# Kernel tuning notes

Measured on AMD Instinct MI355X. Metric: run time of the kernel, lower is better.

## Reference

```python
import jax, jax.numpy as jnp
import numpy as np

B, L, D, H = 4, 2048, 1024, 16
HD = D // H  # head dim = 64


def setup_inputs() -> dict:
    key = jax.random.key(0)
    ks = jax.random.split(key, 8)
    std_qkv = np.sqrt(D + D // H).astype(np.float32)  # matches nn.init.normal_ std in source
    xav = np.sqrt(2.0 / (D + D)).astype(np.float32)   # xavier_normal_ for fc_out
    return {
        "query": jax.random.normal(ks[0], (B, L, D), dtype=jnp.float32),
        "key": jax.random.normal(ks[1], (B, L, D), dtype=jnp.float32),
        "value": jax.random.normal(ks[2], (B, L, D), dtype=jnp.float32),
        "Wq": jax.random.normal(ks[3], (D, D), dtype=jnp.float32) * std_qkv,
        "Wk": jax.random.normal(ks[4], (D, D), dtype=jnp.float32) * std_qkv,
        "Wv": jax.random.normal(ks[5], (D, D), dtype=jnp.float32) * std_qkv,
        "Wo": jax.random.normal(ks[6], (D, D), dtype=jnp.float32) * xav,
        "bo": jnp.zeros((D,), dtype=jnp.float32),
    }


def reference(query, key, value, Wq, Wk, Wv, Wo, bo):
    # Linear projections (torch Linear: x @ W.T), then split heads: b l (h k) -> b h l k
    def split_heads(x):
        b, l, _ = x.shape
        return x.reshape(b, l, H, HD).transpose(0, 2, 1, 3)

    q = split_heads(query @ Wq.T)   # [B,H,L,HD]
    k = split_heads(key @ Wk.T)     # [B,H,T,HD]
    v = split_heads(value @ Wv.T)   # [B,H,T,HD]

    scale = 1.0 / np.sqrt(HD).astype(np.float32)
    energy = jnp.einsum("bhlk,bhtk->bhlt", q, k) * scale  # [B,H,L,T]
    attention = jax.nn.softmax(energy, axis=3)
    out = jnp.einsum("bhlt,bhtv->bhlv", attention, v)     # [B,H,L,HD]
    # b h l v -> b l (h v)
    out = out.transpose(0, 2, 1, 3).reshape(B, L, D)
    out = out @ Wo.T + bo  # dropout_rate=0.0 -> identity
    return out, attention
```

## Files before the change

### kernel.cpp

```cpp
#include <hip/hip_runtime.h>
#include <math.h>

#define Bb 4
#define Ls 2048
#define Dd 1024
#define Hh 16
#define HDm 64
#define ML (Bb*Ls)

typedef double f64x4 __attribute__((ext_vector_type(4)));
typedef unsigned int u32;

__device__ __forceinline__ void gload16(const void* g, void* l) {
  __builtin_amdgcn_global_load_lds(
      (const __attribute__((address_space(1))) u32*)g,
      (__attribute__((address_space(3))) u32*)l, 16, 0, 0);
}

__global__ __launch_bounds__(256) void gemm_nt_mfma_f64(
    const float* __restrict__ A, const float* __restrict__ B,
    double* __restrict__ C, double outscale) {
  const int N = Dd, K = Dd;
  __shared__ float As[64][17];
  __shared__ float Bs[64][17];
  const int tid = threadIdx.x;
  const int lane = tid & 63;
  const int w = tid >> 6;
  const int lrow = lane & 15, lk = lane >> 4;
  const int bm = blockIdx.y * 64, bn = blockIdx.x * 64;
  const int sr = tid >> 4, sc = tid & 15;

  f64x4 acc[4] = {{0.,0.,0.,0.},{0.,0.,0.,0.},{0.,0.,0.,0.},{0.,0.,0.,0.}};

  for (int k0 = 0; k0 < K; k0 += 16) {
#pragma unroll
    for (int i = 0; i < 4; i++) {
      int r = sr + 16 * i;
      As[r][sc] = A[(size_t)(bm + r) * K + k0 + sc];
      Bs[r][sc] = B[(size_t)(bn + r) * K + k0 + sc];
    }
    __syncthreads();
#pragma unroll
    for (int t = 0; t < 4; t++) {
      double a = (double)As[16 * w + lrow][4 * t + lk];
#pragma unroll
      for (int j = 0; j < 4; j++) {
        double bb = (double)Bs[16 * j + lrow][4 * t + lk];
        acc[j] = __builtin_amdgcn_mfma_f64_16x16x4f64(a, bb, acc[j], 0, 0, 0);
      }
    }
    __syncthreads();
  }
#pragma unroll
  for (int j = 0; j < 4; j++)
#pragma unroll
    for (int d = 0; d < 4; d++) {
      size_t m = (size_t)(bm + 16 * w + 4 * d + lk);
      C[m * N + bn + 16 * j + lrow] = acc[j][d] * outscale;
    }
}

__global__ __launch_bounds__(256) void gemm_nt_mfma_f32(
    const float* __restrict__ A, const float* __restrict__ B,
    const float* __restrict__ bias, float* __restrict__ C) {
  const int N = Dd, K = Dd;
  __shared__ float As[64][17];
  __shared__ float Bs[64][17];
  const int tid = threadIdx.x;
  const int lane = tid & 63;
  const int w = tid >> 6;
  const int lrow = lane & 15, lk = lane >> 4;
  const int bm = blockIdx.y * 64, bn = blockIdx.x * 64;
  const int sr = tid >> 4, sc = tid & 15;

  f64x4 acc[4] = {{0.,0.,0.,0.},{0.,0.,0.,0.},{0.,0.,0.,0.},{0.,0.,0.,0.}};

  for (int k0 = 0; k0 < K; k0 += 16) {
#pragma unroll
    for (int i = 0; i < 4; i++) {
      int r = sr + 16 * i;
      As[r][sc] = A[(size_t)(bm + r) * K + k0 + sc];
      Bs[r][sc] = B[(size_t)(bn + r) * K + k0 + sc];
    }
    __syncthreads();
#pragma unroll
    for (int t = 0; t < 4; t++) {
      double a = (double)As[16 * w + lrow][4 * t + lk];
#pragma unroll
      for (int j = 0; j < 4; j++) {
        double bb = (double)Bs[16 * j + lrow][4 * t + lk];
        acc[j] = __builtin_amdgcn_mfma_f64_16x16x4f64(a, bb, acc[j], 0, 0, 0);
      }
    }
    __syncthreads();
  }
#pragma unroll
  for (int j = 0; j < 4; j++)
#pragma unroll
    for (int d = 0; d < 4; d++) {
      size_t m = (size_t)(bm + 16 * w + 4 * d + lk);
      int n = bn + 16 * j + lrow;
      float v = (float)acc[j][d];
      if (bias) v += bias[n];
      C[m * N + n] = v;
    }
}

__global__ __launch_bounds__(256) void attn_flash(
    double* __restrict__ Qd, const double* __restrict__ Kd,
    const float* __restrict__ Vf, float* __restrict__ attn,
    float* __restrict__ O) {
  __shared__ double Kbuf[2][32 * 64];
  __shared__ float  Vbuf[2][32 * 64];
  __shared__ float  Ps[4][32 * 20];

  const int tid = threadIdx.x;
  const int lane = tid & 63;
  const int w = tid >> 6;
  const int lrow = lane & 15;
  const int lk = lane >> 4;
  const int blk = blockIdx.x;
  const int qt = blk & 31;
  const int h = (blk >> 5) & 15;
  const int b = blk >> 9;
  const int l0 = qt * 64;

  const double* Qg = Qd + ((size_t)(b * Ls + l0)) * Dd + h * HDm;
  const double* Kg = Kd + ((size_t)b * Ls) * Dd + h * HDm;
  const float*  Vg = Vf + ((size_t)b * Ls) * Dd + h * HDm;
  float* aout = attn + ((size_t)((b * Hh + h) * Ls + l0)) * Ls;

  double qreg[16];
#pragma unroll
  for (int t = 0; t < 16; t++)
    qreg[t] = Qg[(size_t)(16 * w + lrow) * Dd + 4 * t + lk];

  const int l16 = (lane & 31) * 16;
  const int halfk = lane >> 5;
  const int vin = (lane & 15) * 16;
  const int vrow = lane >> 4;
  const int sx = (lrow & 7) << 1;

  auto stage = [&](int kts, int bsel) {
#pragma unroll
    for (int jj = 0; jj < 4; jj++) {
      int i = w + 4 * jj;
      int row = 2 * i + halfk;
      int inner = l16 ^ ((row & 7) << 4);
      const char* g = (const char*)Kg + (((size_t)(kts * 32 + row)) << 13) + inner;
      gload16(g, (char*)(&Kbuf[bsel][0]) + i * 1024);
    }
#pragma unroll
    for (int jj = 0; jj < 2; jj++) {
      int j = w + 4 * jj;
      int row = 4 * j + vrow;
      const char* g = (const char*)Vg + (((size_t)(kts * 32 + row)) << 12) + vin;
      gload16(g, (char*)(&Vbuf[bsel][0]) + j * 1024);
    }
  };

  float mreff[4];
  double sacc[4];
  float Oacc[4][4];
#pragma unroll
  for (int d = 0; d < 4; d++) {
    mreff[d] = -INFINITY;
    sacc[d] = 0.0;
#pragma unroll
    for (int j = 0; j < 4; j++) Oacc[d][j] = 0.0f;
  }

  stage(0, 0);
  __syncthreads();

  int cur = 0;
  for (int kt = 0; kt < 64; kt++) {
    if (kt < 63) stage(kt + 1, cur ^ 1);

    const double* Kb = &Kbuf[cur][0];
    const float*  Vb = &Vbuf[cur][0];

    f64x4 acc0 = {0.0, 0.0, 0.0, 0.0};
    f64x4 acc1 = {0.0, 0.0, 0.0, 0.0};
#pragma unroll
    for (int t = 0; t < 16; t++) {
      int ko = (4 * t + lk) ^ sx;
      double b0 = Kb[lrow * 64 + ko];
      double b1 = Kb[(16 + lrow) * 64 + ko];
      acc0 = __builtin_amdgcn_mfma_f64_16x16x4f64(qreg[t], b0, acc0, 0, 0, 0);
      acc1 = __builtin_amdgcn_mfma_f64_16x16x4f64(qreg[t], b1, acc1, 0, 0, 0);
    }

#pragma unroll
    for (int d = 0; d < 4; d++) {
      double e0 = acc0[d];
      double e1 = acc1[d];
      float tmf = fmaxf((float)e0, (float)e1);
#pragma unroll
      for (int m = 1; m < 16; m <<= 1) tmf = fmaxf(tmf, __shfl_xor(tmf, m));
      float mo_f = mreff[d];
      float ref_f = fmaxf(mo_f, tmf);
      double ref = (double)ref_f;
      float p0 = expf((float)(e0 - ref));
      float p1 = expf((float)(e1 - ref));
      double ts = (double)p0 + (double)p1;
#pragma unroll
      for (int m = 1; m < 16; m <<= 1) ts += __shfl_xor(ts, m);
      float factor = expf(mo_f - ref_f);
      sacc[d] = sacc[d] * (double)factor + ts;
      mreff[d] = ref_f;
#pragma unroll
      for (int j = 0; j < 4; j++) Oacc[d][j] *= factor;
      int row = 16 * w + 4 * d + lk;
      aout[(size_t)row * Ls + kt * 32 + lrow] = p0;
      aout[(size_t)row * Ls + kt * 32 + 16 + lrow] = p1;
      if (lrow == 0) {
        ((float*)(Qd + ((size_t)(b * Ls + l0 + row)) * Dd + h * HDm))[kt] = ref_f;
      }
      Ps[w][lrow * 20 + 4 * lk + d] = p0;
      Ps[w][(16 + lrow) * 20 + 4 * lk + d] = p1;
    }

#pragma unroll
    for (int t = 0; t < 32; t++) {
      float4 pb = *(const float4*)(&Ps[w][t * 20 + 4 * lk]);
      float4 vv = *(const float4*)(&Vb[t * 64 + lrow * 4]);
      Oacc[0][0] = fmaf(pb.x, vv.x, Oacc[0][0]);
      Oacc[0][1] = fmaf(pb.x, vv.y, Oacc[0][1]);
      Oacc[0][2] = fmaf(pb.x, vv.z, Oacc[0][2]);
      Oacc[0][3] = fmaf(pb.x, vv.w, Oacc[0][3]);
      Oacc[1][0] = fmaf(pb.y, vv.x, Oacc[1][0]);
      Oacc[1][1] = fmaf(pb.y, vv.y, Oacc[1][1]);
      Oacc[1][2] = fmaf(pb.y, vv.z, Oacc[1][2]);
      Oacc[1][3] = fmaf(pb.y, vv.w, Oacc[1][3]);
      Oacc[2][0] = fmaf(pb.z, vv.x, Oacc[2][0]);
      Oacc[2][1] = fmaf(pb.z, vv.y, Oacc[2][1]);
      Oacc[2][2] = fmaf(pb.z, vv.z, Oacc[2][2]);
      Oacc[2][3] = fmaf(pb.z, vv.w, Oacc[2][3]);
      Oacc[3][0] = fmaf(pb.w, vv.x, Oacc[3][0]);
      Oacc[3][1] = fmaf(pb.w, vv.y, Oacc[3][1]);
      Oacc[3][2] = fmaf(pb.w, vv.z, Oacc[3][2]);
      Oacc[3][3] = fmaf(pb.w, vv.w, Oacc[3][3]);
    }

    __syncthreads();
    cur ^= 1;
  }

#pragma unroll
  for (int d = 0; d < 4; d++) {
    int row = 16 * w + 4 * d + lk;
    float sv = (float)(1.0 / sacc[d]);
    float4 ov = make_float4(Oacc[d][0] * sv, Oacc[d][1] * sv,
                            Oacc[d][2] * sv, Oacc[d][3] * sv);
    *(float4*)(O + ((size_t)(b * Ls + l0 + row)) * Dd + h * HDm + lrow * 4) = ov;
    if (lrow == 0) {
      float* mrow = (float*)(Qd + ((size_t)(b * Ls + l0 + row)) * Dd + h * HDm);
      mrow[64] = mreff[d];
      *(double*)(mrow + 66) = sacc[d];
    }
  }
}

__global__ __launch_bounds__(256) void attn_scale(
    float* __restrict__ attn, const double* __restrict__ Qd) {
  int R = blockIdx.x;
  int b = R >> 15;
  int rem = R & 32767;
  int h = rem >> 11;
  int l = rem & 2047;
  const float* mrow = (const float*)(Qd + ((size_t)(b * Ls + l)) * Dd + h * HDm);
  int tid = threadIdx.x;
  int kt = tid >> 2;
  double mt = (double)mrow[kt];
  double mf = (double)mrow[64];
  double s = *(const double*)(mrow + 66);
  float sc = (float)(exp(mt - mf) / s);
  float4* ap = (float4*)(attn + (size_t)R * Ls + tid * 8);
  float4 a0 = ap[0], a1 = ap[1];
  a0.x *= sc; a0.y *= sc; a0.z *= sc; a0.w *= sc;
  a1.x *= sc; a1.y *= sc; a1.z *= sc; a1.w *= sc;
  ap[0] = a0; ap[1] = a1;
}

extern "C" void kernel_launch(void* const* d_in, const int* in_sizes, int n_in,
                              void* d_out, int out_size, void* d_ws, size_t ws_size,
                              hipStream_t stream) {
  const float* query = (const float*)d_in[0];
  const float* key   = (const float*)d_in[1];
  const float* value = (const float*)d_in[2];
  const float* Wq    = (const float*)d_in[3];
  const float* Wk    = (const float*)d_in[4];
  const float* Wv    = (const float*)d_in[5];
  const float* Wo    = (const float*)d_in[6];
  const float* bo    = (const float*)d_in[7];

  float* out0 = (float*)d_out;
  float* attn = out0 + (size_t)ML * Dd;

  char* ws = (char*)d_ws;
  double* Qd = (double*)ws;
  double* Kd = (double*)(ws + (size_t)ML * Dd * 8);
  float*  Vf = (float*)(ws + (size_t)ML * Dd * 16);
  float*  Of = (float*)(ws + (size_t)ML * Dd * 16 + (size_t)ML * Dd * 4);

  dim3 gemm_grid(Dd / 64, ML / 64);
  gemm_nt_mfma_f64<<<gemm_grid, 256, 0, stream>>>(query, Wq, Qd, 0.125);
  gemm_nt_mfma_f64<<<gemm_grid, 256, 0, stream>>>(key,   Wk, Kd, 1.0);
  gemm_nt_mfma_f32<<<gemm_grid, 256, 0, stream>>>(value, Wv, nullptr, Vf);

  attn_flash<<<Bb * Hh * (Ls / 64), 256, 0, stream>>>(Qd, Kd, Vf, attn, Of);
  attn_scale<<<Bb * Hh * Ls, 256, 0, stream>>>(attn, Qd);

  gemm_nt_mfma_f32<<<gemm_grid, 256, 0, stream>>>(Of, Wo, bo, out0);
}
```

Baseline: 4.203 ms.

## Compute P·V with bf16 MFMA using bf16-stored V projection

The V projection now writes its output as bf16 instead of fp32, and the attention kernel's P·V product moves from scalar FMA loops to bf16 16x16x32 MFMA instructions. P is packed to bf16 in shared memory, and the per-row rescale factors pass through a small shared buffer. This is meant to cut VALU work and V load bandwidth in the flash loop. In exchange it lowers the precision of V and P in the output accumulation, and it reads the V fragment with strided scalar LDS loads.

```diff
diff --git a/kernel.cpp b/kernel.cpp
--- a/kernel.cpp
+++ b/kernel.cpp
@@ -9,12 +9,21 @@
 #define ML (Bb*Ls)
 
 typedef double f64x4 __attribute__((ext_vector_type(4)));
+typedef float  f32x4 __attribute__((ext_vector_type(4)));
+typedef short  bf16x8 __attribute__((ext_vector_type(8)));
 typedef unsigned int u32;
+typedef unsigned short u16;
 
 __device__ __forceinline__ void gload16(const void* g, void* l) {
   __builtin_amdgcn_global_load_lds(
       (const __attribute__((address_space(1))) u32*)g,
       (__attribute__((address_space(3))) u32*)l, 16, 0, 0);
+}
+
+__device__ __forceinline__ u16 f2bf(float f) {
+  u32 u = __float_as_uint(f);
+  u += 0x7FFFu + ((u >> 16) & 1u);
+  return (u16)(u >> 16);
 }
 
 __global__ __launch_bounds__(256) void gemm_nt_mfma_f64(
@@ -106,13 +115,57 @@
     }
 }
 
+__global__ __launch_bounds__(256) void gemm_nt_mfma_bf16o(
+    const float* __restrict__ A, const float* __restrict__ B,
+    u16* __restrict__ C) {
+  const int N = Dd, K = Dd;
+  __shared__ float As[64][17];
+  __shared__ float Bs[64][17];
+  const int tid = threadIdx.x;
+  const int lane = tid & 63;
+  const int w = tid >> 6;
+  const int lrow = lane & 15, lk = lane >> 4;
+  const int bm = blockIdx.y * 64, bn = blockIdx.x * 64;
+  const int sr = tid >> 4, sc = tid & 15;
+
+  f64x4 acc[4] = {{0.,0.,0.,0.},{0.,0.,0.,0.},{0.,0.,0.,0.},{0.,0.,0.,0.}};
+
+  for (int k0 = 0; k0 < K; k0 += 16) {
+#pragma unroll
+    for (int i = 0; i < 4; i++) {
+      int r = sr + 16 * i;
+      As[r][sc] = A[(size_t)(bm + r) * K + k0 + sc];
+      Bs[r][sc] = B[(size_t)(bn + r) * K + k0 + sc];
+    }
+    __syncthreads();
+#pragma unroll
+    for (int t = 0; t < 4; t++) {
+      double a = (double)As[16 * w + lrow][4 * t + lk];
+#pragma unroll
+      for (int j = 0; j < 4; j++) {
+        double bb = (double)Bs[16 * j + lrow][4 * t + lk];
+        acc[j] = __builtin_amdgcn_mfma_f64_16x16x4f64(a, bb, acc[j], 0, 0, 0);
+      }
+    }
+    __syncthreads();
+  }
+#pragma unroll
+  for (int j = 0; j < 4; j++)
+#pragma unroll
+    for (int d = 0; d < 4; d++) {
+      size_t m = (size_t)(bm + 16 * w + 4 * d + lk);
+      C[m * N + bn + 16 * j + lrow] = f2bf((float)acc[j][d]);
+    }
+}
+
 __global__ __launch_bounds__(256) void attn_flash(
     double* __restrict__ Qd, const double* __restrict__ Kd,
-    const float* __restrict__ Vf, float* __restrict__ attn,
+    const u16* __restrict__ Vf, float* __restrict__ attn,
     float* __restrict__ O) {
-  __shared__ double Kbuf[2][32 * 64];
-  __shared__ float  Vbuf[2][32 * 64];
-  __shared__ float  Ps[4][32 * 20];
+  __shared__ __align__(16) double Kbuf[2][32 * 64];
+  __shared__ __align__(16) u16    Vb16[2][32 * 64];
+  __shared__ __align__(16) u16    Pb[4][16 * 32];
+  __shared__ __align__(16) float  Fs[4][16];
 
   const int tid = threadIdx.x;
   const int lane = tid & 63;
@@ -127,7 +180,7 @@
 
   const double* Qg = Qd + ((size_t)(b * Ls + l0)) * Dd + h * HDm;
   const double* Kg = Kd + ((size_t)b * Ls) * Dd + h * HDm;
-  const float*  Vg = Vf + ((size_t)b * Ls) * Dd + h * HDm;
+  const u16*    Vg = Vf + ((size_t)b * Ls) * Dd + h * HDm;
   float* aout = attn + ((size_t)((b * Hh + h) * Ls + l0)) * Ls;
 
   double qreg[16];
@@ -137,8 +190,6 @@
 
   const int l16 = (lane & 31) * 16;
   const int halfk = lane >> 5;
-  const int vin = (lane & 15) * 16;
-  const int vrow = lane >> 4;
   const int sx = (lrow & 7) << 1;
 
   auto stage = [&](int kts, int bsel) {
@@ -150,24 +201,21 @@
       const char* g = (const char*)Kg + (((size_t)(kts * 32 + row)) << 13) + inner;
       gload16(g, (char*)(&Kbuf[bsel][0]) + i * 1024);
     }
-#pragma unroll
-    for (int jj = 0; jj < 2; jj++) {
-      int j = w + 4 * jj;
-      int row = 4 * j + vrow;
-      const char* g = (const char*)Vg + (((size_t)(kts * 32 + row)) << 12) + vin;
-      gload16(g, (char*)(&Vbuf[bsel][0]) + j * 1024);
+    {
+      const char* g = (const char*)Vg +
+          ((size_t)(kts * 32 + 8 * w + (lane >> 3))) * (Dd * 2) + (lane & 7) * 16;
+      gload16(g, (char*)(&Vb16[bsel][0]) + w * 1024);
     }
   };
 
   float mreff[4];
   double sacc[4];
-  float Oacc[4][4];
+  f32x4 pacc[4];
 #pragma unroll
   for (int d = 0; d < 4; d++) {
     mreff[d] = -INFINITY;
     sacc[d] = 0.0;
-#pragma unroll
-    for (int j = 0; j < 4; j++) Oacc[d][j] = 0.0f;
+    pacc[d] = (f32x4){0.f, 0.f, 0.f, 0.f};
   }
 
   stage(0, 0);
@@ -178,7 +226,6 @@
     if (kt < 63) stage(kt + 1, cur ^ 1);
 
     const double* Kb = &Kbuf[cur][0];
-    const float*  Vb = &Vbuf[cur][0];
 
     f64x4 acc0 = {0.0, 0.0, 0.0, 0.0};
     f64x4 acc1 = {0.0, 0.0, 0.0, 0.0};
@@ -209,52 +256,54 @@
       float factor = expf(mo_f - ref_f);
       sacc[d] = sacc[d] * (double)factor + ts;
       mreff[d] = ref_f;
-#pragma unroll
-      for (int j = 0; j < 4; j++) Oacc[d][j] *= factor;
       int row = 16 * w + 4 * d + lk;
       aout[(size_t)row * Ls + kt * 32 + lrow] = p0;
       aout[(size_t)row * Ls + kt * 32 + 16 + lrow] = p1;
       if (lrow == 0) {
         ((float*)(Qd + ((size_t)(b * Ls + l0 + row)) * Dd + h * HDm))[kt] = ref_f;
+        Fs[w][4 * d + lk] = factor;
       }
-      Ps[w][lrow * 20 + 4 * lk + d] = p0;
-      Ps[w][(16 + lrow) * 20 + 4 * lk + d] = p1;
-    }
-
-#pragma unroll
-    for (int t = 0; t < 32; t++) {
-      float4 pb = *(const float4*)(&Ps[w][t * 20 + 4 * lk]);
-      float4 vv = *(const float4*)(&Vb[t * 64 + lrow * 4]);
-      Oacc[0][0] = fmaf(pb.x, vv.x, Oacc[0][0]);
-      Oacc[0][1] = fmaf(pb.x, vv.y, Oacc[0][1]);
-      Oacc[0][2] = fmaf(pb.x, vv.z, Oacc[0][2]);
-      Oacc[0][3] = fmaf(pb.x, vv.w, Oacc[0][3]);
-      Oacc[1][0] = fmaf(pb.y, vv.x, Oacc[1][0]);
-      Oacc[1][1] = fmaf(pb.y, vv.y, Oacc[1][1]);
-      Oacc[1][2] = fmaf(pb.y, vv.z, Oacc[1][2]);
-      Oacc[1][3] = fmaf(pb.y, vv.w, Oacc[1][3]);
-      Oacc[2][0] = fmaf(pb.z, vv.x, Oacc[2][0]);
-      Oacc[2][1] = fmaf(pb.z, vv.y, Oacc[2][1]);
-      Oacc[2][2] = fmaf(pb.z, vv.z, Oacc[2][2]);
-      Oacc[2][3] = fmaf(pb.z, vv.w, Oacc[2][3]);
-      Oacc[3][0] = fmaf(pb.w, vv.x, Oacc[3][0]);
-      Oacc[3][1] = fmaf(pb.w, vv.y, Oacc[3][1]);
-      Oacc[3][2] = fmaf(pb.w, vv.z, Oacc[3][2]);
-      Oacc[3][3] = fmaf(pb.w, vv.w, Oacc[3][3]);
+      Pb[w][(4 * d + lk) * 32 + lrow] = f2bf(p0);
+      Pb[w][(4 * d + lk) * 32 + 16 + lrow] = f2bf(p1);
+    }
+
+    bf16x8 afr = *(const bf16x8*)&Pb[w][lrow * 32 + 8 * lk];
+    f32x4 fv = *(const f32x4*)&Fs[w][4 * lk];
+    const u16* Vb = &Vb16[cur][0];
+#pragma unroll
+    for (int q = 0; q < 4; q++) {
+      pacc[q][0] *= fv[0];
+      pacc[q][1] *= fv[1];
+      pacc[q][2] *= fv[2];
+      pacc[q][3] *= fv[3];
+      bf16x8 bfr;
+#pragma unroll
+      for (int r = 0; r < 8; r++)
+        bfr[r] = (short)Vb[(8 * lk + r) * 64 + 16 * q + lrow];
+      pacc[q] = __builtin_amdgcn_mfma_f32_16x16x32_bf16(afr, bfr, pacc[q], 0, 0, 0);
     }
 
     __syncthreads();
     cur ^= 1;
   }
 
-#pragma unroll
-  for (int d = 0; d < 4; d++) {
-    int row = 16 * w + 4 * d + lk;
-    float sv = (float)(1.0 / sacc[d]);
-    float4 ov = make_float4(Oacc[d][0] * sv, Oacc[d][1] * sv,
-                            Oacc[d][2] * sv, Oacc[d][3] * sv);
-    *(float4*)(O + ((size_t)(b * Ls + l0 + row)) * Dd + h * HDm + lrow * 4) = ov;
-    if (lrow == 0) {
+  if (lrow == 0) {
+#pragma unroll
+    for (int d = 0; d < 4; d++) Fs[w][4 * d + lk] = (float)(1.0 / sacc[d]);
+  }
+  f32x4 sv = *(const f32x4*)&Fs[w][4 * lk];
+#pragma unroll
+  for (int q = 0; q < 4; q++)
+#pragma unroll
+    for (int r = 0; r < 4; r++) {
+      int row = 16 * w + 4 * lk + r;
+      O[((size_t)(b * Ls + l0 + row)) * Dd + h * HDm + 16 * q + lrow] =
+          pacc[q][r] * sv[r];
+    }
+  if (lrow == 0) {
+#pragma unroll
+    for (int d = 0; d < 4; d++) {
+      int row = 16 * w + 4 * d + lk;
       float* mrow = (float*)(Qd + ((size_t)(b * Ls + l0 + row)) * Dd + h * HDm);
       mrow[64] = mreff[d];
       *(double*)(mrow + 66) = sacc[d];
@@ -299,17 +348,17 @@
   float* attn = out0 + (size_t)ML * Dd;
 
   char* ws = (char*)d_ws;
-  double* Qd = (double*)ws;
-  double* Kd = (double*)(ws + (size_t)ML * Dd * 8);
-  float*  Vf = (float*)(ws + (size_t)ML * Dd * 16);
-  float*  Of = (float*)(ws + (size_t)ML * Dd * 16 + (size_t)ML * Dd * 4);
+  double* Qd  = (double*)ws;
+  double* Kd  = (double*)(ws + (size_t)ML * Dd * 8);
+  u16*    Vfb = (u16*)(ws + (size_t)ML * Dd * 16);
+  float*  Of  = (float*)(ws + (size_t)ML * Dd * 16 + (size_t)ML * Dd * 2);
 
   dim3 gemm_grid(Dd / 64, ML / 64);
   gemm_nt_mfma_f64<<<gemm_grid, 256, 0, stream>>>(query, Wq, Qd, 0.125);
   gemm_nt_mfma_f64<<<gemm_grid, 256, 0, stream>>>(key,   Wk, Kd, 1.0);
-  gemm_nt_mfma_f32<<<gemm_grid, 256, 0, stream>>>(value, Wv, nullptr, Vf);
-
-  attn_flash<<<Bb * Hh * (Ls / 64), 256, 0, stream>>>(Qd, Kd, Vf, attn, Of);
+  gemm_nt_mfma_bf16o<<<gemm_grid, 256, 0, stream>>>(value, Wv, Vfb);
+
+  attn_flash<<<Bb * Hh * (Ls / 64), 256, 0, stream>>>(Qd, Kd, Vfb, attn, Of);
   attn_scale<<<Bb * Hh * Ls, 256, 0, stream>>>(attn, Qd);
 
   gemm_nt_mfma_f32<<<gemm_grid, 256, 0, stream>>>(Of, Wo, bo, out0);
```

Result: faster. 3.972 ms (-5.5%).
